# Optimization experiments

Measured on AMD Instinct MI355X. Metric: run time of the kernel, lower is better.

Reference implementation:

```python
import jax, jax.numpy as jnp
import numpy as np

N_HEAD = 16
COND_LEN = 256  # n_unmasked; mask[i, j] == 1 iff j < COND_LEN + i


def rotate_half(x):
    # interleaved pairs: (x0, x1, x2, x3, ...) -> (-x1, x0, -x3, x2, ...)
    x = x.reshape(x.shape[:-1] + (-1, 2))
    x1, x2 = x[..., 0], x[..., 1]
    return jnp.stack([-x2, x1], axis=-1).reshape(x.shape[:-2] + (-1,))


def apply_rotary_pos_emb(t, freqs):
    # t: [B, H, T, l], freqs: [T, l] -> broadcast over B, H
    return t * jnp.cos(freqs) + rotate_half(t) * jnp.sin(freqs)


def setup_inputs() -> dict:
    key = jax.random.key(0)
    ks = jax.random.split(key, 12)
    B, T, C = 8, 769, 1024
    l = 32
    s = 0.02
    return {
        "x_q": jax.random.normal(ks[0], (B, T, C), jnp.float32),
        "x_kv": jax.random.normal(ks[1], (B, T, C), jnp.float32),
        "rotary_pos_emb": jax.random.uniform(ks[2], (T, l), jnp.float32),
        "Wq": jax.random.normal(ks[3], (C, C), jnp.float32) * s,
        "bq": jnp.zeros((C,), jnp.float32),
        "Wk": jax.random.normal(ks[4], (C, C), jnp.float32) * s,
        "bk": jnp.zeros((C,), jnp.float32),
        "Wv": jax.random.normal(ks[5], (C, C), jnp.float32) * s,
        "bv": jnp.zeros((C,), jnp.float32),
        "Wp": jax.random.normal(ks[6], (C, C), jnp.float32) * s,
        "bp": jnp.zeros((C,), jnp.float32),
    }


def reference(x_q, x_kv, rotary_pos_emb, Wq, bq, Wk, bk, Wv, bv, Wp, bp):
    B, T_q, C = x_q.shape
    T_kv = x_kv.shape[1]
    H = N_HEAD
    hd = C // H

    def heads(x, W, b, T):
        return (x @ W.T + b).reshape(B, T, H, hd).transpose(0, 2, 1, 3)  # [B,H,T,hd]

    q = heads(x_q, Wq, bq, T_q)
    k = heads(x_kv, Wk, bk, T_kv)
    v = heads(x_kv, Wv, bv, T_kv)

    # partial rotary on first l dims of q and k
    l = rotary_pos_emb.shape[-1]
    q = jnp.concatenate([apply_rotary_pos_emb(q[..., :l], rotary_pos_emb), q[..., l:]], axis=-1)
    k = jnp.concatenate([apply_rotary_pos_emb(k[..., :l], rotary_pos_emb), k[..., l:]], axis=-1)

    att = jnp.einsum("bhqd,bhkd->bhqk", q, k) * (1.0 / jnp.sqrt(jnp.asarray(hd, q.dtype)))
    # custom prefix+causal mask: allowed iff col < COND_LEN + row
    row = jnp.arange(T_q)[:, None]
    col = jnp.arange(T_kv)[None, :]
    allowed = col < (COND_LEN + row)  # [T_q, T_kv]
    att = jnp.where(allowed[None, None], att, -jnp.inf)
    att = jax.nn.softmax(att, axis=-1)

    y = jnp.einsum("bhqk,bhkd->bhqd", att, v)
    y = y.transpose(0, 2, 1, 3).reshape(B, T_q, C)
    return y @ Wp.T + bp
```

## Files before the change

### kernel.cpp

```cpp
#include <hip/hip_runtime.h>
#include <stdint.h>

#define B_    8
#define T_    769
#define C_    1024
#define H_    16
#define COND_ 256
#define NTOK  (B_*T_)
#define BH_   (B_*H_)
#define TP_   896

typedef short    v8s  __attribute__((ext_vector_type(8)));
typedef float    v4f  __attribute__((ext_vector_type(4)));
typedef uint16_t u16x4 __attribute__((ext_vector_type(4)));
typedef uint16_t u16x8 __attribute__((ext_vector_type(8)));

__device__ __forceinline__ uint16_t f2bf(float f) {
  uint32_t u = __builtin_bit_cast(uint32_t, f);
  u += 0x7fffu + ((u >> 16) & 1u);
  return (uint16_t)(u >> 16);
}
__device__ __forceinline__ float bf2f(uint16_t h) {
  uint32_t u = ((uint32_t)h) << 16;
  return __builtin_bit_cast(float, u);
}

__device__ __forceinline__ void gl_lds16(const void* gptr, void* lptr) {
  __builtin_amdgcn_global_load_lds(
      (const __attribute__((address_space(1))) uint32_t*)gptr,
      (__attribute__((address_space(3))) uint32_t*)lptr,
      16, 0, 0);
}

__device__ __forceinline__ int xcd_swz_bij(int orig, int nwg) {
  int q = nwg >> 3, r = nwg & 7;
  int xcd = orig & 7;
  int base = (xcd < r) ? xcd * (q + 1) : r * (q + 1) + (xcd - r) * q;
  return base + (orig >> 3);
}

__global__ __launch_bounds__(256) void convert_bf16(
    const float* xq, const float* xkv, const float* wq, const float* wk,
    const float* wv, const float* wp,
    uint16_t* dxq, uint16_t* dxkv, uint16_t* dwq, uint16_t* dwk,
    uint16_t* dwv, uint16_t* dwp)
{
  int bid = blockIdx.x;
  const float* s; uint16_t* d; int base;
  if (bid < 6152)       { s = xq;  d = dxq;  base = bid; }
  else if (bid < 12304) { s = xkv; d = dxkv; base = bid - 6152; }
  else {
    int r = bid - 12304;
    int wsel = r >> 10; base = r & 1023;
    s = (wsel == 0) ? wq : (wsel == 1) ? wk : (wsel == 2) ? wv : wp;
    d = (wsel == 0) ? dwq : (wsel == 1) ? dwk : (wsel == 2) ? dwv : dwp;
  }
  int i = base * 256 + threadIdx.x;
  float4 f = ((const float4*)s)[i];
  u16x4 o;
  o[0] = f2bf(f.x); o[1] = f2bf(f.y); o[2] = f2bf(f.z); o[3] = f2bf(f.w);
  ((u16x4*)d)[i] = o;
}


__device__ __forceinline__ void gemm_stage64(
    const uint16_t* const Aptr[4], const uint16_t* const Bptr[4],
    int k0, uint16_t* sA, uint16_t* sB, int tid)
{
  #pragma unroll
  for (int r = 0; r < 4; r++) {
    gl_lds16(Aptr[r] + k0, sA + (r * 256 + tid) * 8);
    gl_lds16(Bptr[r] + k0, sB + (r * 256 + tid) * 8);
  }
}

__device__ __forceinline__ void gemm_compute64(
    const uint16_t* sAc, const uint16_t* sBc, v4f acc[4][4],
    int rbase, int cbase, int quad, int l15)
{
  #pragma unroll
  for (int s = 0; s < 2; s++) {
    v8s af[4], bfv[4];
    #pragma unroll
    for (int i = 0; i < 4; i++) {
      int m = rbase + i * 16 + l15;
      af[i] = *(const v8s*)(sAc + m * 64 + (((s * 4 + quad) ^ (m & 7)) * 8));
    }
    #pragma unroll
    for (int j = 0; j < 4; j++) {
      int n = cbase + j * 16 + l15;
      bfv[j] = *(const v8s*)(sBc + n * 64 + (((s * 4 + quad) ^ (n & 7)) * 8));
    }
    #pragma unroll
    for (int i = 0; i < 4; i++)
      #pragma unroll
      for (int j = 0; j < 4; j++)
        acc[i][j] = __builtin_amdgcn_mfma_f32_16x16x32_bf16(af[i], bfv[j], acc[i][j], 0, 0, 0);
  }
}

__device__ __forceinline__ void gemm_mainloop64(
    const uint16_t* A, const uint16_t* W, int M, int row0, int col0,
    v4f acc[4][4], uint16_t* sA, uint16_t* sB)
{
  const int tid = threadIdx.x;
  const int lane = tid & 63, w = tid >> 6, quad = lane >> 4, l15 = lane & 15;
  const int rbase = (w >> 1) * 64, cbase = (w & 1) * 64;

  const uint16_t* Aptr[4];
  const uint16_t* Bptr[4];
  #pragma unroll
  for (int r = 0; r < 4; r++) {
    int c = r * 256 + tid;
    int row = c >> 3, qp = c & 7;
    int g = qp ^ (row & 7);
    Aptr[r] = A + (size_t)min(row0 + row, M - 1) * 1024 + g * 8;
    Bptr[r] = W + (size_t)(col0 + row) * 1024 + g * 8;
  }

  #pragma unroll
  for (int i = 0; i < 4; i++)
    #pragma unroll
    for (int j = 0; j < 4; j++) acc[i][j] = (v4f)0.0f;

  uint16_t* sA0 = sA;         uint16_t* sB0 = sB;
  uint16_t* sA1 = sA + 8192;  uint16_t* sB1 = sB + 8192;

  gemm_stage64(Aptr, Bptr, 0,  sA0, sB0, tid);
  gemm_stage64(Aptr, Bptr, 64, sA1, sB1, tid);

  #pragma unroll 1
  for (int t = 0; t < 16; t++) {
    if (t < 15) {
      asm volatile("s_waitcnt vmcnt(8)" ::: "memory");
    } else {
      asm volatile("s_waitcnt vmcnt(0)" ::: "memory");
    }
    __builtin_amdgcn_s_barrier();
    asm volatile("" ::: "memory");
    uint16_t* cA = (t & 1) ? sA1 : sA0;
    uint16_t* cB = (t & 1) ? sB1 : sB0;
    gemm_compute64(cA, cB, acc, rbase, cbase, quad, l15);
    asm volatile("s_waitcnt lgkmcnt(0)" ::: "memory");
    __builtin_amdgcn_s_barrier();
    asm volatile("" ::: "memory");
    if (t + 2 < 16)
      gemm_stage64(Aptr, Bptr, (t + 2) * 64, cA, cB, tid);
  }
}

__global__ __launch_bounds__(256) void gemm_qkv(
    const uint16_t* xq, const uint16_t* xkv, const uint16_t* Wqkv,
    const float* bq, const float* bk, const float* bv, const float* freqs,
    uint16_t* Q, uint16_t* K, uint16_t* V)
{
  __shared__ uint16_t sA[2 * 128 * 64];
  __shared__ uint16_t sB[2 * 128 * 64];
  const int swz = xcd_swz_bij(blockIdx.x, 1176);
  const int ct = swz % 24, rt = swz / 24;
  const int z = ct >> 3;
  const int col0 = ct * 128, row0 = rt * 128;
  const uint16_t* A = (z == 0) ? xq : xkv;
  const float* bias  = (z == 0) ? bq : (z == 1 ? bk : bv);
  uint16_t* dst      = (z == 0) ? Q  : (z == 1 ? K  : V);

  v4f acc[4][4];
  gemm_mainloop64(A, Wqkv, NTOK, row0, col0, acc, sA, sB);

  const int tid = threadIdx.x;
  const int lane = tid & 63, w = tid >> 6, quad = lane >> 4, l15 = lane & 15;
  const int rbase = (w >> 1) * 64, cbase = (w & 1) * 64;
  #pragma unroll
  for (int i = 0; i < 4; i++) {
    #pragma unroll
    for (int reg = 0; reg < 4; reg++) {
      int n = row0 + rbase + i * 16 + quad * 4 + reg;
      bool ok = (n < NTOK);
      int nn = min(n, NTOK - 1);
      int b = nn / T_, t = nn % T_;
      float vj[4];
      #pragma unroll
      for (int j = 0; j < 4; j++)
        vj[j] = acc[i][j][reg] + bias[(col0 + cbase + j * 16 + l15) & 1023];
      if (z < 2) {
        float v0 = vj[0], v1 = vj[1];
        float p0 = __shfl_xor(v0, 1);
        float p1 = __shfl_xor(v1, 1);
        float f0 = freqs[t * 32 + l15];
        float f1 = freqs[t * 32 + 16 + l15];
        float s0, c0, s1, c1;
        __sincosf(f0, &s0, &c0);
        __sincosf(f1, &s1, &c1);
        if (l15 & 1) { vj[0] = v0 * c0 + p0 * s0; vj[1] = v1 * c1 + p1 * s1; }
        else         { vj[0] = v0 * c0 - p0 * s0; vj[1] = v1 * c1 - p1 * s1; }
      }
      if (z == 0) {
        #pragma unroll
        for (int j = 0; j < 4; j++) vj[j] *= 0.125f;
      }
      if (ok) {
        #pragma unroll
        for (int j = 0; j < 4; j++) {
          int col = col0 + cbase + j * 16 + l15;
          int h = (col >> 6) & 15, d = col & 63;
          dst[((size_t)(b * H_ + h) * T_ + t) * 64 + d] = f2bf(vj[j]);
        }
      }
    }
  }
}

__global__ __launch_bounds__(256) void gemm_out(
    const uint16_t* Y, const uint16_t* wp, const float* bp, float* out)
{
  __shared__ uint16_t sA[2 * 128 * 64];
  __shared__ uint16_t sB[2 * 128 * 64];
  const int swz = xcd_swz_bij(blockIdx.x, 392);
  const int ct = swz & 7, rt = swz >> 3;
  const int col0 = ct * 128, row0 = rt * 128;
  v4f acc[4][4];
  gemm_mainloop64(Y, wp, NTOK, row0, col0, acc, sA, sB);

  const int tid = threadIdx.x;
  const int lane = tid & 63, w = tid >> 6, quad = lane >> 4, l15 = lane & 15;
  const int rbase = (w >> 1) * 64, cbase = (w & 1) * 64;
  #pragma unroll
  for (int i = 0; i < 4; i++) {
    #pragma unroll
    for (int reg = 0; reg < 4; reg++) {
      int n = row0 + rbase + i * 16 + quad * 4 + reg;
      if (n < NTOK) {
        #pragma unroll
        for (int j = 0; j < 4; j++) {
          int col = col0 + cbase + j * 16 + l15;
          out[(size_t)n * 1024 + col] = acc[i][j][reg] + bp[col];
        }
      }
    }
  }
}

__global__ __launch_bounds__(256) void transpose_v(const uint16_t* Vb, uint16_t* Vt)
{
  __shared__ uint16_t sT[64 * 64];
  const int tid = threadIdx.x;
  const int t0 = blockIdx.x * 64, bh = blockIdx.y;
  const uint16_t* src = Vb + (size_t)bh * T_ * 64;
  #pragma unroll
  for (int r = 0; r < 2; r++) {
    int task = r * 256 + tid;
    int t = task >> 3, oc = task & 7;
    int gt = min(t0 + t, T_ - 1);
    u16x8 v = *(const u16x8*)(src + (size_t)gt * 64 + oc * 8);
    int p = oc ^ (t & 7) ^ ((t >> 3) & 7);
    *(u16x8*)(sT + t * 64 + p * 8) = v;
  }
  __syncthreads();
  uint16_t* dst = Vt + (size_t)bh * 64 * TP_;
  #pragma unroll
  for (int r = 0; r < 2; r++) {
    int task = r * 256 + tid;
    int o = task & 7, d = task >> 3;
    u16x8 v;
    #pragma unroll
    for (int k = 0; k < 8; k++) {
      int t = o * 8 + k;
      int p = (d >> 3) ^ k ^ o;
      v[k] = sT[t * 64 + p * 8 + (d & 7)];
    }
    *(u16x8*)(dst + (size_t)d * TP_ + t0 + o * 8) = v;
  }
}

__global__ __launch_bounds__(256) void attn(
    const uint16_t* Q, const uint16_t* K, const uint16_t* Vt, uint16_t* Y)
{
  __shared__ uint16_t sK[128 * 64];
  __shared__ uint16_t sVT[64 * 128];
  __shared__ uint16_t sP[4 * 16 * 136];

  const int tid = threadIdx.x;
  const int lane = tid & 63, w = tid >> 6, quad = lane >> 4, l15 = lane & 15;
  const int swz = xcd_swz_bij(blockIdx.x, 1664);
  const int qt = swz % 13, bh = swz / 13;
  const int b = bh >> 4, h = bh & 15;
  const int q0 = qt * 64;

  const uint16_t* Qb = Q + (size_t)bh * T_ * 64;
  const uint16_t* Kb = K + (size_t)bh * T_ * 64;
  const uint16_t* Vtb = Vt + (size_t)bh * 64 * TP_;

  const int qr = min(q0 + w * 16 + l15, T_ - 1);
  v8s aq0 = *(const v8s*)(Qb + (size_t)qr * 64 + quad * 8);
  v8s aq1 = *(const v8s*)(Qb + (size_t)qr * 64 + 32 + quad * 8);

  float l_r[4] = {0.f, 0.f, 0.f, 0.f};
  v4f o[4];
  #pragma unroll
  for (int r = 0; r < 4; r++) o[r] = (v4f)0.0f;

  const int kend = min(T_, q0 + 319);
  const int nkt = (kend + 127) >> 7;

  #define STAGE_K(K0)                                                     \
    {                                                                     \
      _Pragma("unroll")                                                   \
      for (int r = 0; r < 4; r++) {                                       \
        int c = r * 256 + tid;                                            \
        int key = c >> 3, qp = c & 7;                                     \
        int g = qp ^ (key & 7);                                           \
        int gk = min((K0) + key, T_ - 1);                                 \
        gl_lds16(Kb + (size_t)gk * 64 + g * 8, sK + c * 8);               \
      }                                                                   \
    }
  #define STAGE_V(K0)                                                     \
    {                                                                     \
      _Pragma("unroll")                                                   \
      for (int r = 0; r < 4; r++) {                                       \
        int c = r * 256 + tid;                                            \
        int d = c >> 4, p = c & 15;                                       \
        int g = (p & 8) | ((p ^ d) & 7);                                  \
        gl_lds16(Vtb + (size_t)d * TP_ + (K0) + g * 8, sVT + c * 8);      \
      }                                                                   \
    }

  STAGE_K(0);
  STAGE_V(0);

  for (int kt = 0; kt < nkt; kt++) {
    const int k0 = kt * 128;
    asm volatile("s_waitcnt vmcnt(4)" ::: "memory");
    __builtin_amdgcn_s_barrier();
    asm volatile("" ::: "memory");

    v4f s[8];
    #pragma unroll
    for (int cb = 0; cb < 8; cb++) {
      int key_l = cb * 16 + l15;
      v8s b0 = *(const v8s*)(sK + (key_l * 8 + ((quad) ^ (key_l & 7))) * 8);
      v8s b1 = *(const v8s*)(sK + (key_l * 8 + ((4 + quad) ^ (key_l & 7))) * 8);
      v4f zz = (v4f)0.0f;
      zz = __builtin_amdgcn_mfma_f32_16x16x32_bf16(aq0, b0, zz, 0, 0, 0);
      zz = __builtin_amdgcn_mfma_f32_16x16x32_bf16(aq1, b1, zz, 0, 0, 0);
      s[cb] = zz;
    }

    uint16_t* pw = sP + w * (16 * 136);
    const int qrow_base = q0 + w * 16 + quad * 4;
    const bool full = (k0 + 128 <= COND_ + q0) && (k0 + 128 <= T_);
    if (full) {
      #pragma unroll
      for (int reg = 0; reg < 4; reg++) {
        float rs = 0.f;
        #pragma unroll
        for (int cb = 0; cb < 8; cb++) {
          float pv = __expf(s[cb][reg]);
          uint16_t pb = f2bf(pv);
          rs += bf2f(pb);
          pw[(quad * 4 + reg) * 136 + cb * 16 + l15] = pb;
        }
        #pragma unroll
        for (int off = 1; off < 16; off <<= 1) rs += __shfl_xor(rs, off);
        l_r[reg] += rs;
      }
    } else {
      #pragma unroll
      for (int reg = 0; reg < 4; reg++) {
        int lim = min(COND_ + qrow_base + reg, T_);
        float rs = 0.f;
        #pragma unroll
        for (int cb = 0; cb < 8; cb++) {
          int key = k0 + cb * 16 + l15;
          float pv = (key < lim) ? __expf(s[cb][reg]) : 0.f;
          uint16_t pb = f2bf(pv);
          rs += bf2f(pb);
          pw[(quad * 4 + reg) * 136 + cb * 16 + l15] = pb;
        }
        #pragma unroll
        for (int off = 1; off < 16; off <<= 1) rs += __shfl_xor(rs, off);
        l_r[reg] += rs;
      }
    }

    asm volatile("s_waitcnt vmcnt(0)" ::: "memory");
    __builtin_amdgcn_s_barrier();
    asm volatile("" ::: "memory");
    if (kt + 1 < nkt) STAGE_K(k0 + 128);

    #pragma unroll
    for (int ks = 0; ks < 4; ks++) {
      v8s ap = *(const v8s*)(pw + l15 * 136 + ks * 32 + quad * 8);
      #pragma unroll
      for (int cbd = 0; cbd < 4; cbd++) {
        int d = cbd * 16 + l15;
        v8s bv = *(const v8s*)(sVT + d * 128 + (((ks * 4 + quad) ^ (d & 7)) * 8));
        o[cbd] = __builtin_amdgcn_mfma_f32_16x16x32_bf16(ap, bv, o[cbd], 0, 0, 0);
      }
    }

    asm volatile("s_waitcnt lgkmcnt(0)" ::: "memory");
    __builtin_amdgcn_s_barrier();
    asm volatile("" ::: "memory");
    if (kt + 1 < nkt) STAGE_V(k0 + 128);
  }
  #undef STAGE_K
  #undef STAGE_V

  #pragma unroll
  for (int reg = 0; reg < 4; reg++) {
    int t = q0 + w * 16 + quad * 4 + reg;
    if (t < T_) {
      float inv = 1.0f / l_r[reg];
      #pragma unroll
      for (int cbd = 0; cbd < 4; cbd++) {
        int d = cbd * 16 + l15;
        Y[((size_t)(b * T_ + t)) * C_ + h * 64 + d] = f2bf(o[cbd][reg] * inv);
      }
    }
  }
}

extern "C" void kernel_launch(void* const* d_in, const int* in_sizes, int n_in,
                              void* d_out, int out_size, void* d_ws, size_t ws_size,
                              hipStream_t stream)
{
  const float* x_q   = (const float*)d_in[0];
  const float* x_kv  = (const float*)d_in[1];
  const float* freqs = (const float*)d_in[2];
  const float* Wq = (const float*)d_in[3];
  const float* bq = (const float*)d_in[4];
  const float* Wk = (const float*)d_in[5];
  const float* bk = (const float*)d_in[6];
  const float* Wv = (const float*)d_in[7];
  const float* bv = (const float*)d_in[8];
  const float* Wp = (const float*)d_in[9];
  const float* bp = (const float*)d_in[10];
  float* out = (float*)d_out;

  const size_t SZX = (size_t)NTOK * C_;
  const size_t SZW = (size_t)C_ * C_;
  uint16_t* ws = (uint16_t*)d_ws;
  uint16_t* xq_bf  = ws;
  uint16_t* xkv_bf = xq_bf + SZX;
  uint16_t* wq_bf  = xkv_bf + SZX;
  uint16_t* wk_bf  = wq_bf + SZW;
  uint16_t* wv_bf  = wk_bf + SZW;
  uint16_t* wp_bf  = wv_bf + SZW;
  uint16_t* Qb = wp_bf + SZW;
  uint16_t* Kb = Qb + SZX;
  uint16_t* Vb = Kb + SZX;
  uint16_t* Vt = ws;
  uint16_t* Yb = Vb;

  convert_bf16<<<dim3(16400), 256, 0, stream>>>(
      x_q, x_kv, Wq, Wk, Wv, Wp, xq_bf, xkv_bf, wq_bf, wk_bf, wv_bf, wp_bf);

  gemm_qkv<<<dim3(1176), 256, 0, stream>>>(
      xq_bf, xkv_bf, wq_bf, bq, bk, bv, freqs, Qb, Kb, Vb);

  transpose_v<<<dim3(13, BH_), 256, 0, stream>>>(Vb, Vt);

  attn<<<dim3(1664), 256, 0, stream>>>(Qb, Kb, Vt, Yb);

  gemm_out<<<dim3(392), 256, 0, stream>>>(Yb, wp_bf, bp, out);
}
```

Measured before the change: 274.5 us.

## Keep attention probabilities in registers via transposed QK MFMA and lane shuffles

The QK^T MFMA now takes its operands swapped, so each lane holds scores for a single query row across 4 consecutive keys. Probabilities are packed as bf16 pairs in registers and rearranged into the PV MFMA A-operand layout with cross-lane shuffles, which removes the per-wave shared-memory P buffer and its LDS writes and reads. The row-sum reduction also shrinks to two shuffles. The cost is sixteen ds_bpermute-style shuffles per k-step plus selects, and more live registers.

```diff
diff --git a/kernel.cpp b/kernel.cpp
--- a/kernel.cpp
+++ b/kernel.cpp
@@ -14,6 +14,7 @@
 typedef float    v4f  __attribute__((ext_vector_type(4)));
 typedef uint16_t u16x4 __attribute__((ext_vector_type(4)));
 typedef uint16_t u16x8 __attribute__((ext_vector_type(8)));
+typedef uint32_t u32x4 __attribute__((ext_vector_type(4)));
 
 __device__ __forceinline__ uint16_t f2bf(float f) {
   uint32_t u = __builtin_bit_cast(uint32_t, f);
@@ -277,7 +278,6 @@
 {
   __shared__ uint16_t sK[128 * 64];
   __shared__ uint16_t sVT[64 * 128];
-  __shared__ uint16_t sP[4 * 16 * 136];
 
   const int tid = threadIdx.x;
   const int lane = tid & 63, w = tid >> 6, quad = lane >> 4, l15 = lane & 15;
@@ -290,17 +290,23 @@
   const uint16_t* Kb = K + (size_t)bh * T_ * 64;
   const uint16_t* Vtb = Vt + (size_t)bh * 64 * TP_;
 
-  const int qr = min(q0 + w * 16 + l15, T_ - 1);
+  const int qa = q0 + w * 16 + l15;
+  const int lim = min(COND_ + qa, T_);
+  const int qr = min(qa, T_ - 1);
   v8s aq0 = *(const v8s*)(Qb + (size_t)qr * 64 + quad * 8);
   v8s aq1 = *(const v8s*)(Qb + (size_t)qr * 64 + 32 + quad * 8);
 
-  float l_r[4] = {0.f, 0.f, 0.f, 0.f};
+  float l_r = 0.f;
   v4f o[4];
   #pragma unroll
   for (int r = 0; r < 4; r++) o[r] = (v4f)0.0f;
 
   const int kend = min(T_, q0 + 319);
   const int nkt = (kend + 127) >> 7;
+
+  const int srcA = (((quad << 1)    ) & 3) * 16 + l15;
+  const int srcB = (((quad << 1) + 1) & 3) * 16 + l15;
+  const bool hiq = (quad >= 2);
 
   #define STAGE_K(K0)                                                     \
     {                                                                     \
@@ -340,47 +346,42 @@
       v8s b0 = *(const v8s*)(sK + (key_l * 8 + ((quad) ^ (key_l & 7))) * 8);
       v8s b1 = *(const v8s*)(sK + (key_l * 8 + ((4 + quad) ^ (key_l & 7))) * 8);
       v4f zz = (v4f)0.0f;
-      zz = __builtin_amdgcn_mfma_f32_16x16x32_bf16(aq0, b0, zz, 0, 0, 0);
-      zz = __builtin_amdgcn_mfma_f32_16x16x32_bf16(aq1, b1, zz, 0, 0, 0);
+      zz = __builtin_amdgcn_mfma_f32_16x16x32_bf16(b0, aq0, zz, 0, 0, 0);
+      zz = __builtin_amdgcn_mfma_f32_16x16x32_bf16(b1, aq1, zz, 0, 0, 0);
       s[cb] = zz;
     }
 
-    uint16_t* pw = sP + w * (16 * 136);
-    const int qrow_base = q0 + w * 16 + quad * 4;
+    uint32_t pk01[8], pk23[8];
+    float rs = 0.f;
     const bool full = (k0 + 128 <= COND_ + q0) && (k0 + 128 <= T_);
     if (full) {
       #pragma unroll
-      for (int reg = 0; reg < 4; reg++) {
-        float rs = 0.f;
-        #pragma unroll
-        for (int cb = 0; cb < 8; cb++) {
-          float pv = __expf(s[cb][reg]);
-          uint16_t pb = f2bf(pv);
-          rs += bf2f(pb);
-          pw[(quad * 4 + reg) * 136 + cb * 16 + l15] = pb;
-        }
-        #pragma unroll
-        for (int off = 1; off < 16; off <<= 1) rs += __shfl_xor(rs, off);
-        l_r[reg] += rs;
+      for (int cb = 0; cb < 8; cb++) {
+        uint16_t pb0 = f2bf(__expf(s[cb][0]));
+        uint16_t pb1 = f2bf(__expf(s[cb][1]));
+        uint16_t pb2 = f2bf(__expf(s[cb][2]));
+        uint16_t pb3 = f2bf(__expf(s[cb][3]));
+        pk01[cb] = (uint32_t)pb0 | ((uint32_t)pb1 << 16);
+        pk23[cb] = (uint32_t)pb2 | ((uint32_t)pb3 << 16);
+        rs += bf2f(pb0) + bf2f(pb1) + bf2f(pb2) + bf2f(pb3);
       }
     } else {
       #pragma unroll
-      for (int reg = 0; reg < 4; reg++) {
-        int lim = min(COND_ + qrow_base + reg, T_);
-        float rs = 0.f;
-        #pragma unroll
-        for (int cb = 0; cb < 8; cb++) {
-          int key = k0 + cb * 16 + l15;
-          float pv = (key < lim) ? __expf(s[cb][reg]) : 0.f;
-          uint16_t pb = f2bf(pv);
-          rs += bf2f(pb);
-          pw[(quad * 4 + reg) * 136 + cb * 16 + l15] = pb;
-        }
-        #pragma unroll
-        for (int off = 1; off < 16; off <<= 1) rs += __shfl_xor(rs, off);
-        l_r[reg] += rs;
-      }
-    }
+      for (int cb = 0; cb < 8; cb++) {
+        int keyb = k0 + cb * 16 + quad * 4;
+        float p0 = (keyb + 0 < lim) ? __expf(s[cb][0]) : 0.f;
+        float p1 = (keyb + 1 < lim) ? __expf(s[cb][1]) : 0.f;
+        float p2 = (keyb + 2 < lim) ? __expf(s[cb][2]) : 0.f;
+        float p3 = (keyb + 3 < lim) ? __expf(s[cb][3]) : 0.f;
+        uint16_t pb0 = f2bf(p0), pb1 = f2bf(p1), pb2 = f2bf(p2), pb3 = f2bf(p3);
+        pk01[cb] = (uint32_t)pb0 | ((uint32_t)pb1 << 16);
+        pk23[cb] = (uint32_t)pb2 | ((uint32_t)pb3 << 16);
+        rs += bf2f(pb0) + bf2f(pb1) + bf2f(pb2) + bf2f(pb3);
+      }
+    }
+    rs += __shfl_xor(rs, 16);
+    rs += __shfl_xor(rs, 32);
+    l_r += rs;
 
     asm volatile("s_waitcnt vmcnt(0)" ::: "memory");
     __builtin_amdgcn_s_barrier();
@@ -389,7 +390,17 @@
 
     #pragma unroll
     for (int ks = 0; ks < 4; ks++) {
-      v8s ap = *(const v8s*)(pw + l15 * 136 + ks * 32 + quad * 8);
+      const int cbE = 2 * ks, cbO = 2 * ks + 1;
+      uint32_t a01E = __shfl((int)pk01[cbE], srcA), a01O = __shfl((int)pk01[cbO], srcA);
+      uint32_t a23E = __shfl((int)pk23[cbE], srcA), a23O = __shfl((int)pk23[cbO], srcA);
+      uint32_t b01E = __shfl((int)pk01[cbE], srcB), b01O = __shfl((int)pk01[cbO], srcB);
+      uint32_t b23E = __shfl((int)pk23[cbE], srcB), b23O = __shfl((int)pk23[cbO], srcB);
+      u32x4 pw;
+      pw[0] = hiq ? a01O : a01E;
+      pw[1] = hiq ? a23O : a23E;
+      pw[2] = hiq ? b01O : b01E;
+      pw[3] = hiq ? b23O : b23E;
+      v8s ap = __builtin_bit_cast(v8s, pw);
       #pragma unroll
       for (int cbd = 0; cbd < 4; cbd++) {
         int d = cbd * 16 + l15;
@@ -408,9 +419,11 @@
 
   #pragma unroll
   for (int reg = 0; reg < 4; reg++) {
-    int t = q0 + w * 16 + quad * 4 + reg;
+    int r_ = quad * 4 + reg;
+    float lv = __shfl(l_r, (lane & 48) | r_);
+    int t = q0 + w * 16 + r_;
     if (t < T_) {
-      float inv = 1.0f / l_r[reg];
+      float inv = 1.0f / lv;
       #pragma unroll
       for (int cbd = 0; cbd < 4; cbd++) {
         int d = cbd * 16 + l15;
```

Measured after the change: 277.9 us. Within noise of the previous version (+1.2%).
